# Performance work log

Hardware: AMD Instinct MI355X
Metric: run time of the kernel (lower is better)

Reference implementation:

```python
import jax, jax.numpy as jnp
import numpy as np

N = 40000
E = 640000
IN_F, HID, OUT_F = 128, 128, 64


def setup_inputs() -> dict:
    key = jax.random.key(0)
    ks = jax.random.split(key, 6)
    x = jax.random.normal(ks[0], (N, IN_F), dtype=jnp.float32)
    edge_index = jax.random.randint(ks[1], (2, E), 0, N, dtype=jnp.int64)
    s_in = 1.0 / np.sqrt(IN_F)
    s_hid = 1.0 / np.sqrt(HID)
    W1l = jax.random.normal(ks[2], (IN_F, HID), dtype=jnp.float32) * s_in
    W1r = jax.random.normal(ks[3], (IN_F, HID), dtype=jnp.float32) * s_in
    b1 = jnp.zeros((HID,), dtype=jnp.float32)
    W2l = jax.random.normal(ks[4], (HID, OUT_F), dtype=jnp.float32) * s_hid
    W2r = jax.random.normal(ks[5], (HID, OUT_F), dtype=jnp.float32) * s_hid
    b2 = jnp.zeros((OUT_F,), dtype=jnp.float32)
    return {"x": x, "edge_index": edge_index, "W1l": W1l, "b1": b1,
            "W1r": W1r, "W2l": W2l, "b2": b2, "W2r": W2r}


def _mean_agg(x, src, dst, n_nodes):
    # mean of source-node features over incoming edges at each destination
    sums = jax.ops.segment_sum(x[src], dst, num_segments=n_nodes)  # [N, D]
    cnt = jax.ops.segment_sum(jnp.ones((src.shape[0],), x.dtype), dst,
                              num_segments=n_nodes)
    return sums / jnp.maximum(cnt, 1.0)[:, None]


def _sage_conv(x, src, dst, Wl, b, Wr, n_nodes):
    # PyG SAGEConv (mean aggr): lin_l(mean_j x_j) + lin_r(x_i), bias in lin_l
    agg = _mean_agg(x, src, dst, n_nodes)
    return agg @ Wl + b + x @ Wr


def reference(x, edge_index, W1l, b1, W1r, W2l, b2, W2r):
    src, dst = edge_index[0], edge_index[1]
    n = x.shape[0]
    h = jax.nn.relu(_sage_conv(x, src, dst, W1l, b1, W1r, n))
    return _sage_conv(h, src, dst, W2l, b2, W2r, n)
```

## Files before the change

kernel.cpp:

```cpp
#include <hip/hip_runtime.h>

#define NNODES 40000
#define NEDGES 640000
#define PAD 64
#define NBK 160
#define BNODES 250
#define BCAP 8192
#define ACHUNK 4000

typedef unsigned int uint32;
typedef unsigned short ushort16;
typedef short bf16x8 __attribute__((ext_vector_type(8)));
typedef float f32x4 __attribute__((ext_vector_type(4)));

static __device__ __forceinline__ ushort16 f2bf(float f) {
    uint32 u = __builtin_bit_cast(uint32, f);
    uint32 r = u + 0x7fffu + ((u >> 16) & 1u);
    return (ushort16)(r >> 16);
}
static __device__ __forceinline__ float bf_lo(uint32 u) {
    uint32 t = u << 16;
    return __builtin_bit_cast(float, t);
}
static __device__ __forceinline__ float bf_hi(uint32 u) {
    uint32 t = u & 0xffff0000u;
    return __builtin_bit_cast(float, t);
}

static __device__ __forceinline__ void acc8(float* s, uint4 u) {
    s[0] += bf_lo(u.x); s[1] += bf_hi(u.x);
    s[2] += bf_lo(u.y); s[3] += bf_hi(u.y);
    s[4] += bf_lo(u.z); s[5] += bf_hi(u.z);
    s[6] += bf_lo(u.w); s[7] += bf_hi(u.w);
}

static __device__ __forceinline__ int edge_val(const void* ep, long long idx, int is64) {
    if (is64) return (int)((const long long*)ep)[idx];
    return ((const int*)ep)[idx];
}

__global__ void prep_kernel(const float* __restrict__ x, uint32* __restrict__ xbf2,
                            int* __restrict__ gcur,
                            const float* __restrict__ W1l, const float* __restrict__ W1r,
                            const float* __restrict__ W2l, const float* __restrict__ W2r,
                            ushort16* __restrict__ Wfrag1, ushort16* __restrict__ Wfrag2,
                            const int* __restrict__ e32, int* __restrict__ flag) {
    int b = blockIdx.x;
    if (b < 5000) {
        int i = b * 256 + threadIdx.x;
        float4 v = ((const float4*)x)[i];
        uint2 o;
        o.x = (uint32)f2bf(v.x) | ((uint32)f2bf(v.y) << 16);
        o.y = (uint32)f2bf(v.z) | ((uint32)f2bf(v.w) << 16);
        ((uint2*)xbf2)[i] = o;
        return;
    }
    int i = (b - 5000) * 256 + threadIdx.x;
    if (i < NBK) gcur[i] = 0;
    if (i == 0) {
        int any = 0;
        for (int t = 0; t < 64; ++t) any |= e32[2 * t + 1];
        *flag = (any == 0) ? 1 : 0;
    }
    if (i < 32768) {
        int j = i & 7, lane = (i >> 3) & 63, nt = (i >> 9) & 7, s = (i >> 12) & 3, by = i >> 14;
        int k = s * 32 + (lane >> 4) * 8 + j;
        int col = nt * 16 + (lane & 15);
        float v = (by == 0) ? W1l[k * 128 + col] : W1r[k * 128 + col];
        Wfrag1[i] = f2bf(v);
    } else {
        int q = i - 32768;
        int j = q & 7, lane = (q >> 3) & 63, nt = (q >> 9) & 7, s = (q >> 12) & 3;
        int k = s * 32 + (lane >> 4) * 8 + j;
        int col = nt * 16 + (lane & 15);
        float v = (col < 64) ? W2l[k * 64 + col] : W2r[k * 64 + (col - 64)];
        Wfrag2[q] = f2bf(v);
    }
}

__global__ __launch_bounds__(256) void buildA_kernel(const void* __restrict__ edges,
                                                     const int* __restrict__ flag,
                                                     int* __restrict__ gcur,
                                                     int* __restrict__ bstream) {
    __shared__ int hist[NBK];
    __shared__ int cur[NBK];
    int tid = threadIdx.x;
    int base = blockIdx.x * ACHUNK;
    for (int i = tid; i < NBK; i += 256) hist[i] = 0;
    __syncthreads();
    int is64 = *flag;
#pragma unroll
    for (int k = 0; k < (ACHUNK + 255) / 256; ++k) {
        int off = k * 256 + tid;
        if (off < ACHUNK) {
            int d = edge_val(edges, (long long)NEDGES + base + off, is64);
            atomicAdd(&hist[d / BNODES], 1);
        }
    }
    __syncthreads();
    if (tid < NBK) cur[tid] = atomicAdd(&gcur[tid], hist[tid]);
    __syncthreads();
#pragma unroll
    for (int k = 0; k < (ACHUNK + 255) / 256; ++k) {
        int off = k * 256 + tid;
        if (off < ACHUNK) {
            int e = base + off;
            int d = edge_val(edges, (long long)NEDGES + e, is64);
            int s = edge_val(edges, e, is64);
            int bk = d / BNODES;
            int dloc = d - bk * BNODES;
            int r = atomicAdd(&cur[bk], 1);
            if (r < BCAP) bstream[bk * BCAP + r] = (s << 8) | dloc;
        }
    }
}

__global__ __launch_bounds__(256) void buildB_kernel(const int* __restrict__ bstream,
                                                     const int* __restrict__ gcur,
                                                     int* __restrict__ cnt,
                                                     int* __restrict__ csr_src) {
    __shared__ int4 img4[BNODES * 16];
    __shared__ int hist[BNODES];
    int* img = (int*)img4;
    int tid = threadIdx.x;
    int bk = blockIdx.x;
    for (int i = tid; i < BNODES; i += 256) hist[i] = 0;
    __syncthreads();
    int n = gcur[bk];
    if (n > BCAP) n = BCAP;
    for (int i = tid; i < n; i += 256) {
        int u = bstream[bk * BCAP + i];
        int dloc = u & 255;
        int s = u >> 8;
        int r = atomicAdd(&hist[dloc], 1);
        if (r < PAD) img[dloc * PAD + r] = s;
    }
    __syncthreads();
    int4* csr4 = (int4*)csr_src;
#pragma unroll
    for (int i = tid; i < BNODES * 16; i += 256) csr4[(size_t)bk * BNODES * 16 + i] = img4[i];
    for (int i = tid; i < BNODES; i += 256) cnt[bk * BNODES + i] = hist[i];
}

__global__ __launch_bounds__(256) void gemm_mfma_kernel(const ushort16* __restrict__ Abf,
                                                        const uint4* __restrict__ WfragG,
                                                        int Lw, int Rw,
                                                        ushort16* __restrict__ bfL,
                                                        ushort16* __restrict__ bfR,
                                                        float* __restrict__ fR) {
    __shared__ uint4 Bs[2048];
    int tid = threadIdx.x;
#pragma unroll
    for (int it = 0; it < 8; ++it) {
        int idx = tid + it * 256;
        Bs[idx] = WfragG[(size_t)blockIdx.y * 2048 + idx];
    }

    int wv = tid >> 6, lane = tid & 63;
    int quad = lane >> 4, c = lane & 15;
    int row0 = blockIdx.x * 64 + wv * 16;

    const uint4* arow = (const uint4*)(Abf + (size_t)(row0 + c) * 128);
    bf16x8 af[4];
#pragma unroll
    for (int s = 0; s < 4; ++s) af[s] = __builtin_bit_cast(bf16x8, arow[s * 4 + quad]);

    __syncthreads();

    f32x4 acc[8];
#pragma unroll
    for (int nt = 0; nt < 8; ++nt) acc[nt] = (f32x4){0.f, 0.f, 0.f, 0.f};

#pragma unroll
    for (int s = 0; s < 4; ++s) {
#pragma unroll
        for (int nt = 0; nt < 8; ++nt) {
            bf16x8 bf = __builtin_bit_cast(bf16x8, Bs[(s * 8 + nt) * 64 + lane]);
            acc[nt] = __builtin_amdgcn_mfma_f32_16x16x32_bf16(af[s], bf, acc[nt], 0, 0, 0);
        }
    }

    int colbase = blockIdx.y * 128;
#pragma unroll
    for (int nt = 0; nt < 8; ++nt) {
        int gcol = colbase + nt * 16 + c;
#pragma unroll
        for (int r = 0; r < 4; ++r) {
            int row = row0 + quad * 4 + r;
            if (gcol < Lw) {
                bfL[(size_t)row * Lw + gcol] = f2bf(acc[nt][r]);
            } else if (bfR) {
                bfR[(size_t)row * Rw + (gcol - Lw)] = f2bf(acc[nt][r]);
            } else {
                fR[(size_t)row * Rw + (gcol - Lw)] = acc[nt][r];
            }
        }
    }
}

__global__ __launch_bounds__(256) void agg1_kernel(const uint4* __restrict__ P4,
                                                   const uint4* __restrict__ S4,
                                                   const int* __restrict__ cnt,
                                                   const int* __restrict__ csr_src,
                                                   const float* __restrict__ b1,
                                                   uint4* __restrict__ hbf4) {
    int wave = threadIdx.x >> 6, lane = threadIdx.x & 63;
    int node = blockIdx.x * 4 + wave;
    if (node >= NNODES) return;
    int c = cnt[node];
    if (c > PAD) c = PAD;
    int beg = node * PAD;
    int sub = lane >> 4;
    int fl = lane & 15;
    float s[8];
#pragma unroll
    for (int i = 0; i < 8; ++i) s[i] = 0.f;

    int idx = 0;
    if (lane < c) idx = csr_src[beg + lane];
    int e = 0;
    for (; e + 8 <= c; e += 8) {
        int a0 = __shfl(idx, e + sub);
        int a1 = __shfl(idx, e + 4 + sub);
        uint4 u0 = P4[(size_t)a0 * 16 + fl];
        uint4 u1 = P4[(size_t)a1 * 16 + fl];
        acc8(s, u0);
        acc8(s, u1);
    }
    for (; e < c; e += 4) {
        int ee = e + sub;
        bool pred = ee < c;
        int a = __shfl(idx, pred ? ee : 0);
        uint4 u = P4[(size_t)a * 16 + fl];
        if (pred) acc8(s, u);
    }
#pragma unroll
    for (int i = 0; i < 8; ++i) s[i] += __shfl_xor(s[i], 16);
#pragma unroll
    for (int i = 0; i < 8; ++i) s[i] += __shfl_xor(s[i], 32);

    if (sub == 0) {
        float ic = 1.0f / (float)(c > 0 ? c : 1);
        uint4 su = S4[(size_t)node * 16 + fl];
        float4 bA = *(const float4*)&b1[fl * 8];
        float4 bB = *(const float4*)&b1[fl * 8 + 4];
        float sv[8];
        sv[0] = bf_lo(su.x); sv[1] = bf_hi(su.x);
        sv[2] = bf_lo(su.y); sv[3] = bf_hi(su.y);
        sv[4] = bf_lo(su.z); sv[5] = bf_hi(su.z);
        sv[6] = bf_lo(su.w); sv[7] = bf_hi(su.w);
        float bb[8] = {bA.x, bA.y, bA.z, bA.w, bB.x, bB.y, bB.z, bB.w};
        float v[8];
#pragma unroll
        for (int i = 0; i < 8; ++i) v[i] = fmaxf(fmaf(s[i], ic, bb[i] + sv[i]), 0.f);
        uint4 o;
        o.x = (uint32)f2bf(v[0]) | ((uint32)f2bf(v[1]) << 16);
        o.y = (uint32)f2bf(v[2]) | ((uint32)f2bf(v[3]) << 16);
        o.z = (uint32)f2bf(v[4]) | ((uint32)f2bf(v[5]) << 16);
        o.w = (uint32)f2bf(v[6]) | ((uint32)f2bf(v[7]) << 16);
        hbf4[(size_t)node * 16 + fl] = o;
    }
}

__global__ __launch_bounds__(256) void agg2_kernel(const uint4* __restrict__ P4,
                                                   const float* __restrict__ selfR2,
                                                   const int* __restrict__ cnt,
                                                   const int* __restrict__ csr_src,
                                                   const float* __restrict__ b2,
                                                   float* __restrict__ out) {
    int wave = threadIdx.x >> 6, lane = threadIdx.x & 63;
    int node = blockIdx.x * 4 + wave;
    if (node >= NNODES) return;
    int c = cnt[node];
    if (c > PAD) c = PAD;
    int beg = node * PAD;
    int sub = lane >> 3;
    int fl = lane & 7;
    float s[8];
#pragma unroll
    for (int i = 0; i < 8; ++i) s[i] = 0.f;

    int idx = 0;
    if (lane < c) idx = csr_src[beg + lane];
    int e = 0;
    for (; e + 16 <= c; e += 16) {
        int a0 = __shfl(idx, e + sub);
        int a1 = __shfl(idx, e + 8 + sub);
        uint4 u0 = P4[(size_t)a0 * 8 + fl];
        uint4 u1 = P4[(size_t)a1 * 8 + fl];
        acc8(s, u0);
        acc8(s, u1);
    }
    for (; e < c; e += 8) {
        int ee = e + sub;
        bool pred = ee < c;
        int a = __shfl(idx, pred ? ee : 0);
        uint4 u = P4[(size_t)a * 8 + fl];
        if (pred) acc8(s, u);
    }
#pragma unroll
    for (int i = 0; i < 8; ++i) s[i] += __shfl_xor(s[i], 8);
#pragma unroll
    for (int i = 0; i < 8; ++i) s[i] += __shfl_xor(s[i], 16);
#pragma unroll
    for (int i = 0; i < 8; ++i) s[i] += __shfl_xor(s[i], 32);

    if (sub == 0) {
        float ic = 1.0f / (float)(c > 0 ? c : 1);
        float4 sA = *(const float4*)&selfR2[(size_t)node * 64 + fl * 8];
        float4 sB = *(const float4*)&selfR2[(size_t)node * 64 + fl * 8 + 4];
        float4 bA = *(const float4*)&b2[fl * 8];
        float4 bB = *(const float4*)&b2[fl * 8 + 4];
        float sv[8] = {sA.x, sA.y, sA.z, sA.w, sB.x, sB.y, sB.z, sB.w};
        float bb[8] = {bA.x, bA.y, bA.z, bA.w, bB.x, bB.y, bB.z, bB.w};
        float v[8];
#pragma unroll
        for (int i = 0; i < 8; ++i) v[i] = fmaf(s[i], ic, bb[i] + sv[i]);
        float4 o0 = make_float4(v[0], v[1], v[2], v[3]);
        float4 o1 = make_float4(v[4], v[5], v[6], v[7]);
        *(float4*)&out[(size_t)node * 64 + fl * 8] = o0;
        *(float4*)&out[(size_t)node * 64 + fl * 8 + 4] = o1;
    }
}

extern "C" void kernel_launch(void* const* d_in, const int* in_sizes, int n_in,
                              void* d_out, int out_size, void* d_ws, size_t ws_size,
                              hipStream_t stream) {
    const float* x   = (const float*)d_in[0];
    const void*  ei  = d_in[1];
    const float* W1l = (const float*)d_in[2];
    const float* b1  = (const float*)d_in[3];
    const float* W1r = (const float*)d_in[4];
    const float* W2l = (const float*)d_in[5];
    const float* b2  = (const float*)d_in[6];
    const float* W2r = (const float*)d_in[7];
    float* out = (float*)d_out;

    char* p = (char*)d_ws;
    auto alloc = [&](size_t bytes) {
        char* r = p;
        p += (bytes + 255) & ~(size_t)255;
        return r;
    };
    int*      flag      = (int*)alloc(4);
    int*      cnt       = (int*)alloc(NNODES * 4);
    int*      gcur      = (int*)alloc(NBK * 4);
    int*      bstream   = (int*)alloc((size_t)NBK * BCAP * 4);
    int*      csr_src   = (int*)alloc((size_t)NNODES * PAD * 4);
    ushort16* Wfrag1    = (ushort16*)alloc(32768 * 2);
    ushort16* Wfrag2    = (ushort16*)alloc(16384 * 2);
    uint32*   xbf       = (uint32*)alloc((size_t)NNODES * 64 * 4);
    ushort16* T1l       = (ushort16*)alloc((size_t)NNODES * 128 * 2);
    ushort16* T1r       = (ushort16*)alloc((size_t)NNODES * 128 * 2);
    uint32*   hbf       = (uint32*)alloc((size_t)NNODES * 64 * 4);
    ushort16* T2l       = (ushort16*)alloc((size_t)NNODES * 64 * 2);
    float*    T2r       = (float*)alloc((size_t)NNODES * 64 * 4);

    prep_kernel<<<5192, 256, 0, stream>>>(x, xbf, gcur, W1l, W1r, W2l, W2r, Wfrag1, Wfrag2,
                                          (const int*)ei, flag);
    buildA_kernel<<<NBK, 256, 0, stream>>>(ei, flag, gcur, bstream);
    buildB_kernel<<<NBK, 256, 0, stream>>>(bstream, gcur, cnt, csr_src);

    gemm_mfma_kernel<<<dim3(NNODES / 64, 2), 256, 0, stream>>>(
        (const ushort16*)xbf, (const uint4*)Wfrag1, 128, 128, T1l, T1r, (float*)nullptr);
    agg1_kernel<<<(NNODES + 3) / 4, 256, 0, stream>>>((const uint4*)T1l, (const uint4*)T1r,
                                                      cnt, csr_src, b1, (uint4*)hbf);

    gemm_mfma_kernel<<<dim3(NNODES / 64, 1), 256, 0, stream>>>(
        (const ushort16*)hbf, (const uint4*)Wfrag2, 64, 64, T2l, (ushort16*)nullptr, T2r);
    agg2_kernel<<<(NNODES + 3) / 4, 256, 0, stream>>>((const uint4*)T2l, T2r, cnt, csr_src, b2,
                                                      out);
}
```

Baseline: 175.6 us.

## Fuse per-bucket CSR build into aggregation kernels and shrink buckets

Removes the separate buildB pass that wrote a padded CSR to global memory. Each aggregation workgroup now rebuilds its own bucket's neighbour lists in shared memory from the edge stream and then aggregates 50 nodes with four waves. Buckets shrink to 50 nodes (800 buckets), and the global bucket cursors are padded apart to reduce atomic contention. The cost is that the shared-memory rebuild runs twice, once in each aggregation, and only 800 workgroups launch in place of 10000, which may limit latency hiding on gather-bound work. Per-bucket capacity of 1280 edges against an average of 800 is a tighter overflow margin than before.

```diff
diff --git a/kernel.cpp b/kernel.cpp
--- a/kernel.cpp
+++ b/kernel.cpp
@@ -3,10 +3,12 @@
 #define NNODES 40000
 #define NEDGES 640000
 #define PAD 64
-#define NBK 160
-#define BNODES 250
-#define BCAP 8192
+#define NBK 800
+#define BNODES 50
+#define BCAP 1280
+#define AWGS 160
 #define ACHUNK 4000
+#define GSTR 16
 
 typedef unsigned int uint32;
 typedef unsigned short ushort16;
@@ -38,6 +40,8 @@
     if (is64) return (int)((const long long*)ep)[idx];
     return ((const int*)ep)[idx];
 }
+
+static __device__ __forceinline__ int imin(int a, int b) { return a < b ? a : b; }
 
 __global__ void prep_kernel(const float* __restrict__ x, uint32* __restrict__ xbf2,
                             int* __restrict__ gcur,
@@ -56,7 +60,7 @@
         return;
     }
     int i = (b - 5000) * 256 + threadIdx.x;
-    if (i < NBK) gcur[i] = 0;
+    if (i < NBK * GSTR) gcur[i] = 0;
     if (i == 0) {
         int any = 0;
         for (int t = 0; t < 64; ++t) any |= e32[2 * t + 1];
@@ -98,7 +102,7 @@
         }
     }
     __syncthreads();
-    if (tid < NBK) cur[tid] = atomicAdd(&gcur[tid], hist[tid]);
+    for (int i = tid; i < NBK; i += 256) cur[i] = atomicAdd(&gcur[i * GSTR], hist[i]);
     __syncthreads();
 #pragma unroll
     for (int k = 0; k < (ACHUNK + 255) / 256; ++k) {
@@ -115,33 +119,6 @@
     }
 }
 
-__global__ __launch_bounds__(256) void buildB_kernel(const int* __restrict__ bstream,
-                                                     const int* __restrict__ gcur,
-                                                     int* __restrict__ cnt,
-                                                     int* __restrict__ csr_src) {
-    __shared__ int4 img4[BNODES * 16];
-    __shared__ int hist[BNODES];
-    int* img = (int*)img4;
-    int tid = threadIdx.x;
-    int bk = blockIdx.x;
-    for (int i = tid; i < BNODES; i += 256) hist[i] = 0;
-    __syncthreads();
-    int n = gcur[bk];
-    if (n > BCAP) n = BCAP;
-    for (int i = tid; i < n; i += 256) {
-        int u = bstream[bk * BCAP + i];
-        int dloc = u & 255;
-        int s = u >> 8;
-        int r = atomicAdd(&hist[dloc], 1);
-        if (r < PAD) img[dloc * PAD + r] = s;
-    }
-    __syncthreads();
-    int4* csr4 = (int4*)csr_src;
-#pragma unroll
-    for (int i = tid; i < BNODES * 16; i += 256) csr4[(size_t)bk * BNODES * 16 + i] = img4[i];
-    for (int i = tid; i < BNODES; i += 256) cnt[bk * BNODES + i] = hist[i];
-}
-
 __global__ __launch_bounds__(256) void gemm_mfma_kernel(const ushort16* __restrict__ Abf,
                                                         const uint4* __restrict__ WfragG,
                                                         int Lw, int Rw,
@@ -200,126 +177,154 @@
 
 __global__ __launch_bounds__(256) void agg1_kernel(const uint4* __restrict__ P4,
                                                    const uint4* __restrict__ S4,
-                                                   const int* __restrict__ cnt,
-                                                   const int* __restrict__ csr_src,
+                                                   const int* __restrict__ bstream,
+                                                   const int* __restrict__ gcur,
                                                    const float* __restrict__ b1,
                                                    uint4* __restrict__ hbf4) {
-    int wave = threadIdx.x >> 6, lane = threadIdx.x & 63;
-    int node = blockIdx.x * 4 + wave;
-    if (node >= NNODES) return;
-    int c = cnt[node];
-    if (c > PAD) c = PAD;
-    int beg = node * PAD;
+    __shared__ int img[BNODES * PAD];
+    __shared__ int hist[BNODES];
+    int tid = threadIdx.x, bk = blockIdx.x;
+    for (int i = tid; i < BNODES; i += 256) hist[i] = 0;
+    __syncthreads();
+    int n = gcur[bk * GSTR];
+    if (n > BCAP) n = BCAP;
+    for (int i = tid; i < n; i += 256) {
+        int u = bstream[bk * BCAP + i];
+        int dl = u & 255;
+        int r = atomicAdd(&hist[dl], 1);
+        if (r < PAD) img[dl * PAD + r] = u >> 8;
+    }
+    __syncthreads();
+
+    int wave = tid >> 6, lane = tid & 63;
     int sub = lane >> 4;
     int fl = lane & 15;
-    float s[8];
-#pragma unroll
-    for (int i = 0; i < 8; ++i) s[i] = 0.f;
-
-    int idx = 0;
-    if (lane < c) idx = csr_src[beg + lane];
-    int e = 0;
-    for (; e + 8 <= c; e += 8) {
-        int a0 = __shfl(idx, e + sub);
-        int a1 = __shfl(idx, e + 4 + sub);
-        uint4 u0 = P4[(size_t)a0 * 16 + fl];
-        uint4 u1 = P4[(size_t)a1 * 16 + fl];
-        acc8(s, u0);
-        acc8(s, u1);
-    }
-    for (; e < c; e += 4) {
-        int ee = e + sub;
-        bool pred = ee < c;
-        int a = __shfl(idx, pred ? ee : 0);
-        uint4 u = P4[(size_t)a * 16 + fl];
-        if (pred) acc8(s, u);
-    }
-#pragma unroll
-    for (int i = 0; i < 8; ++i) s[i] += __shfl_xor(s[i], 16);
-#pragma unroll
-    for (int i = 0; i < 8; ++i) s[i] += __shfl_xor(s[i], 32);
-
-    if (sub == 0) {
-        float ic = 1.0f / (float)(c > 0 ? c : 1);
-        uint4 su = S4[(size_t)node * 16 + fl];
-        float4 bA = *(const float4*)&b1[fl * 8];
-        float4 bB = *(const float4*)&b1[fl * 8 + 4];
-        float sv[8];
-        sv[0] = bf_lo(su.x); sv[1] = bf_hi(su.x);
-        sv[2] = bf_lo(su.y); sv[3] = bf_hi(su.y);
-        sv[4] = bf_lo(su.z); sv[5] = bf_hi(su.z);
-        sv[6] = bf_lo(su.w); sv[7] = bf_hi(su.w);
-        float bb[8] = {bA.x, bA.y, bA.z, bA.w, bB.x, bB.y, bB.z, bB.w};
-        float v[8];
-#pragma unroll
-        for (int i = 0; i < 8; ++i) v[i] = fmaxf(fmaf(s[i], ic, bb[i] + sv[i]), 0.f);
-        uint4 o;
-        o.x = (uint32)f2bf(v[0]) | ((uint32)f2bf(v[1]) << 16);
-        o.y = (uint32)f2bf(v[2]) | ((uint32)f2bf(v[3]) << 16);
-        o.z = (uint32)f2bf(v[4]) | ((uint32)f2bf(v[5]) << 16);
-        o.w = (uint32)f2bf(v[6]) | ((uint32)f2bf(v[7]) << 16);
-        hbf4[(size_t)node * 16 + fl] = o;
+    for (int nl = wave; nl < BNODES; nl += 4) {
+        int node = bk * BNODES + nl;
+        int c = hist[nl];
+        if (c > PAD) c = PAD;
+        int nb = nl * PAD;
+        float s[8];
+#pragma unroll
+        for (int i = 0; i < 8; ++i) s[i] = 0.f;
+
+        for (int e = 0; e < c; e += 16) {
+            int cm1 = c - 1;
+            int e0 = e + sub, e1 = e + 4 + sub, e2 = e + 8 + sub, e3 = e + 12 + sub;
+            int a0 = img[nb + imin(e0, cm1)];
+            int a1 = img[nb + imin(e1, cm1)];
+            int a2 = img[nb + imin(e2, cm1)];
+            int a3 = img[nb + imin(e3, cm1)];
+            uint4 u0 = P4[(size_t)a0 * 16 + fl];
+            uint4 u1 = P4[(size_t)a1 * 16 + fl];
+            uint4 u2 = P4[(size_t)a2 * 16 + fl];
+            uint4 u3 = P4[(size_t)a3 * 16 + fl];
+            if (e0 < c) acc8(s, u0);
+            if (e1 < c) acc8(s, u1);
+            if (e2 < c) acc8(s, u2);
+            if (e3 < c) acc8(s, u3);
+        }
+#pragma unroll
+        for (int i = 0; i < 8; ++i) s[i] += __shfl_xor(s[i], 16);
+#pragma unroll
+        for (int i = 0; i < 8; ++i) s[i] += __shfl_xor(s[i], 32);
+
+        if (sub == 0) {
+            float ic = 1.0f / (float)(c > 0 ? c : 1);
+            uint4 su = S4[(size_t)node * 16 + fl];
+            float4 bA = *(const float4*)&b1[fl * 8];
+            float4 bB = *(const float4*)&b1[fl * 8 + 4];
+            float sv[8];
+            sv[0] = bf_lo(su.x); sv[1] = bf_hi(su.x);
+            sv[2] = bf_lo(su.y); sv[3] = bf_hi(su.y);
+            sv[4] = bf_lo(su.z); sv[5] = bf_hi(su.z);
+            sv[6] = bf_lo(su.w); sv[7] = bf_hi(su.w);
+            float bb[8] = {bA.x, bA.y, bA.z, bA.w, bB.x, bB.y, bB.z, bB.w};
+            float v[8];
+#pragma unroll
+            for (int i = 0; i < 8; ++i) v[i] = fmaxf(fmaf(s[i], ic, bb[i] + sv[i]), 0.f);
+            uint4 o;
+            o.x = (uint32)f2bf(v[0]) | ((uint32)f2bf(v[1]) << 16);
+            o.y = (uint32)f2bf(v[2]) | ((uint32)f2bf(v[3]) << 16);
+            o.z = (uint32)f2bf(v[4]) | ((uint32)f2bf(v[5]) << 16);
+            o.w = (uint32)f2bf(v[6]) | ((uint32)f2bf(v[7]) << 16);
+            hbf4[(size_t)node * 16 + fl] = o;
+        }
     }
 }
 
 __global__ __launch_bounds__(256) void agg2_kernel(const uint4* __restrict__ P4,
                                                    const float* __restrict__ selfR2,
-                                                   const int* __restrict__ cnt,
-                                                   const int* __restrict__ csr_src,
+                                                   const int* __restrict__ bstream,
+                                                   const int* __restrict__ gcur,
                                                    const float* __restrict__ b2,
                                                    float* __restrict__ out) {
-    int wave = threadIdx.x >> 6, lane = threadIdx.x & 63;
-    int node = blockIdx.x * 4 + wave;
-    if (node >= NNODES) return;
-    int c = cnt[node];
-    if (c > PAD) c = PAD;
-    int beg = node * PAD;
+    __shared__ int img[BNODES * PAD];
+    __shared__ int hist[BNODES];
+    int tid = threadIdx.x, bk = blockIdx.x;
+    for (int i = tid; i < BNODES; i += 256) hist[i] = 0;
+    __syncthreads();
+    int n = gcur[bk * GSTR];
+    if (n > BCAP) n = BCAP;
+    for (int i = tid; i < n; i += 256) {
+        int u = bstream[bk * BCAP + i];
+        int dl = u & 255;
+        int r = atomicAdd(&hist[dl], 1);
+        if (r < PAD) img[dl * PAD + r] = u >> 8;
+    }
+    __syncthreads();
+
+    int wave = tid >> 6, lane = tid & 63;
     int sub = lane >> 3;
     int fl = lane & 7;
-    float s[8];
-#pragma unroll
-    for (int i = 0; i < 8; ++i) s[i] = 0.f;
-
-    int idx = 0;
-    if (lane < c) idx = csr_src[beg + lane];
-    int e = 0;
-    for (; e + 16 <= c; e += 16) {
-        int a0 = __shfl(idx, e + sub);
-        int a1 = __shfl(idx, e + 8 + sub);
-        uint4 u0 = P4[(size_t)a0 * 8 + fl];
-        uint4 u1 = P4[(size_t)a1 * 8 + fl];
-        acc8(s, u0);
-        acc8(s, u1);
-    }
-    for (; e < c; e += 8) {
-        int ee = e + sub;
-        bool pred = ee < c;
-        int a = __shfl(idx, pred ? ee : 0);
-        uint4 u = P4[(size_t)a * 8 + fl];
-        if (pred) acc8(s, u);
-    }
-#pragma unroll
-    for (int i = 0; i < 8; ++i) s[i] += __shfl_xor(s[i], 8);
-#pragma unroll
-    for (int i = 0; i < 8; ++i) s[i] += __shfl_xor(s[i], 16);
-#pragma unroll
-    for (int i = 0; i < 8; ++i) s[i] += __shfl_xor(s[i], 32);
-
-    if (sub == 0) {
-        float ic = 1.0f / (float)(c > 0 ? c : 1);
-        float4 sA = *(const float4*)&selfR2[(size_t)node * 64 + fl * 8];
-        float4 sB = *(const float4*)&selfR2[(size_t)node * 64 + fl * 8 + 4];
-        float4 bA = *(const float4*)&b2[fl * 8];
-        float4 bB = *(const float4*)&b2[fl * 8 + 4];
-        float sv[8] = {sA.x, sA.y, sA.z, sA.w, sB.x, sB.y, sB.z, sB.w};
-        float bb[8] = {bA.x, bA.y, bA.z, bA.w, bB.x, bB.y, bB.z, bB.w};
-        float v[8];
-#pragma unroll
-        for (int i = 0; i < 8; ++i) v[i] = fmaf(s[i], ic, bb[i] + sv[i]);
-        float4 o0 = make_float4(v[0], v[1], v[2], v[3]);
-        float4 o1 = make_float4(v[4], v[5], v[6], v[7]);
-        *(float4*)&out[(size_t)node * 64 + fl * 8] = o0;
-        *(float4*)&out[(size_t)node * 64 + fl * 8 + 4] = o1;
+    for (int nl = wave; nl < BNODES; nl += 4) {
+        int node = bk * BNODES + nl;
+        int c = hist[nl];
+        if (c > PAD) c = PAD;
+        int nb = nl * PAD;
+        float s[8];
+#pragma unroll
+        for (int i = 0; i < 8; ++i) s[i] = 0.f;
+
+        for (int e = 0; e < c; e += 32) {
+            int cm1 = c - 1;
+            int e0 = e + sub, e1 = e + 8 + sub, e2 = e + 16 + sub, e3 = e + 24 + sub;
+            int a0 = img[nb + imin(e0, cm1)];
+            int a1 = img[nb + imin(e1, cm1)];
+            int a2 = img[nb + imin(e2, cm1)];
+            int a3 = img[nb + imin(e3, cm1)];
+            uint4 u0 = P4[(size_t)a0 * 8 + fl];
+            uint4 u1 = P4[(size_t)a1 * 8 + fl];
+            uint4 u2 = P4[(size_t)a2 * 8 + fl];
+            uint4 u3 = P4[(size_t)a3 * 8 + fl];
+            if (e0 < c) acc8(s, u0);
+            if (e1 < c) acc8(s, u1);
+            if (e2 < c) acc8(s, u2);
+            if (e3 < c) acc8(s, u3);
+        }
+#pragma unroll
+        for (int i = 0; i < 8; ++i) s[i] += __shfl_xor(s[i], 8);
+#pragma unroll
+        for (int i = 0; i < 8; ++i) s[i] += __shfl_xor(s[i], 16);
+#pragma unroll
+        for (int i = 0; i < 8; ++i) s[i] += __shfl_xor(s[i], 32);
+
+        if (sub == 0) {
+            float ic = 1.0f / (float)(c > 0 ? c : 1);
+            float4 sA = *(const float4*)&selfR2[(size_t)node * 64 + fl * 8];
+            float4 sB = *(const float4*)&selfR2[(size_t)node * 64 + fl * 8 + 4];
+            float4 bA = *(const float4*)&b2[fl * 8];
+            float4 bB = *(const float4*)&b2[fl * 8 + 4];
+            float sv[8] = {sA.x, sA.y, sA.z, sA.w, sB.x, sB.y, sB.z, sB.w};
+            float bb[8] = {bA.x, bA.y, bA.z, bA.w, bB.x, bB.y, bB.z, bB.w};
+            float v[8];
+#pragma unroll
+            for (int i = 0; i < 8; ++i) v[i] = fmaf(s[i], ic, bb[i] + sv[i]);
+            float4 o0 = make_float4(v[0], v[1], v[2], v[3]);
+            float4 o1 = make_float4(v[4], v[5], v[6], v[7]);
+            *(float4*)&out[(size_t)node * 64 + fl * 8] = o0;
+            *(float4*)&out[(size_t)node * 64 + fl * 8 + 4] = o1;
+        }
     }
 }
 
@@ -343,10 +348,8 @@
         return r;
     };
     int*      flag      = (int*)alloc(4);
-    int*      cnt       = (int*)alloc(NNODES * 4);
-    int*      gcur      = (int*)alloc(NBK * 4);
+    int*      gcur      = (int*)alloc((size_t)NBK * GSTR * 4);
     int*      bstream   = (int*)alloc((size_t)NBK * BCAP * 4);
-    int*      csr_src   = (int*)alloc((size_t)NNODES * PAD * 4);
     ushort16* Wfrag1    = (ushort16*)alloc(32768 * 2);
     ushort16* Wfrag2    = (ushort16*)alloc(16384 * 2);
     uint32*   xbf       = (uint32*)alloc((size_t)NNODES * 64 * 4);
@@ -358,16 +361,14 @@
 
     prep_kernel<<<5192, 256, 0, stream>>>(x, xbf, gcur, W1l, W1r, W2l, W2r, Wfrag1, Wfrag2,
                                           (const int*)ei, flag);
-    buildA_kernel<<<NBK, 256, 0, stream>>>(ei, flag, gcur, bstream);
-    buildB_kernel<<<NBK, 256, 0, stream>>>(bstream, gcur, cnt, csr_src);
+    buildA_kernel<<<AWGS, 256, 0, stream>>>(ei, flag, gcur, bstream);
 
     gemm_mfma_kernel<<<dim3(NNODES / 64, 2), 256, 0, stream>>>(
         (const ushort16*)xbf, (const uint4*)Wfrag1, 128, 128, T1l, T1r, (float*)nullptr);
-    agg1_kernel<<<(NNODES + 3) / 4, 256, 0, stream>>>((const uint4*)T1l, (const uint4*)T1r,
-                                                      cnt, csr_src, b1, (uint4*)hbf);
+    agg1_kernel<<<NBK, 256, 0, stream>>>((const uint4*)T1l, (const uint4*)T1r, bstream, gcur,
+                                         b1, (uint4*)hbf);
 
     gemm_mfma_kernel<<<dim3(NNODES / 64, 1), 256, 0, stream>>>(
         (const ushort16*)hbf, (const uint4*)Wfrag2, 64, 64, T2l, (ushort16*)nullptr, T2r);
-    agg2_kernel<<<(NNODES + 3) / 4, 256, 0, stream>>>((const uint4*)T2l, T2r, cnt, csr_src, b2,
-                                                      out);
-}
+    agg2_kernel<<<NBK, 256, 0, stream>>>((const uint4*)T2l, T2r, bstream, gcur, b2, out);
+}
```

After: 185.8 us. 5.8% more time.
